# Kernel tuning notes

Measured on AMD Instinct MI355X. Metric: run time of the kernel, lower is better.

Reference implementation:

```python
import jax, jax.numpy as jnp
import numpy as np
from jax import lax


def binarize(x):
    # sign() binarization with straight-through estimator (identity backward),
    # matching the BNN .data in-place trick in BinarizeConv2d / bilinear.
    return x + lax.stop_gradient(jnp.sign(x) - x)


def maxpool2x2(x):
    # NCHW 2x2 max pool, stride 2
    return lax.reduce_window(x, -jnp.inf, lax.max,
                             (1, 1, 2, 2), (1, 1, 2, 2), 'VALID')


def conv2d(x, w):
    # NCHW / OIHW valid conv, stride 1
    return lax.conv_general_dilated(x, w, (1, 1), 'VALID',
                                    dimension_numbers=('NCHW', 'OIHW', 'NCHW'))


def setup_inputs() -> dict:
    key = jax.random.key(0)
    ks = jax.random.split(key, 6)
    B = 16384
    x = jax.random.normal(ks[0], (B, 1, 32, 32), dtype=jnp.float32)
    w1 = jax.random.normal(ks[1], (6, 1, 5, 5), dtype=jnp.float32) * 0.2
    w2 = jax.random.normal(ks[2], (16, 6, 5, 5), dtype=jnp.float32) * 0.08
    wfc1 = jax.random.normal(ks[3], (120, 400), dtype=jnp.float32) * 0.05
    wfc2 = jax.random.normal(ks[4], (84, 120), dtype=jnp.float32) * 0.09
    wfc3 = jax.random.normal(ks[5], (10, 84), dtype=jnp.float32) * 0.1
    return {'x': x, 'w1': w1, 'w2': w2, 'wfc1': wfc1, 'wfc2': wfc2, 'wfc3': wfc3}


def reference(x, w1, w2, wfc1, wfc2, wfc3):
    # conv1 (binarized input + weights) -> pool
    h = maxpool2x2(conv2d(binarize(x), binarize(w1)))          # [B,6,14,14]
    # conv2 -> pool
    h = maxpool2x2(conv2d(binarize(h), binarize(w2)))          # [B,16,5,5]
    h = h.reshape(h.shape[0], -1)                              # [B,400]
    h = binarize(h) @ binarize(wfc1).T                         # [B,120]
    h = binarize(h) @ binarize(wfc2).T                         # [B,84]
    h = binarize(h) @ binarize(wfc3).T                         # [B,10]
    return h
```

## Files before the change

### kernel.cpp

```cpp
#include <hip/hip_runtime.h>
#include <hip/hip_bf16.h>

typedef unsigned int u32;
typedef unsigned short u16;
typedef unsigned long long u64;

#define OC1 0
#define OC2 8
#define WCONV 104
#define OF1 104
#define OF2 2024
#define OF3 2664
#define WTOT 2704

__global__ void pack_w(const float* __restrict__ w1, const float* __restrict__ w2,
                       const float* __restrict__ f1, const float* __restrict__ f2,
                       const float* __restrict__ f3, u64* __restrict__ P) {
    int g = blockIdx.x * 256 + threadIdx.x;
    if (g < 1920) {
        int j = g / 15, w = g % 15;
        u64 v = 0;
        if (w < 14 && j < 120) {
            bool sp = (w >= 7); int k = sp ? w - 7 : w;
            for (int f = 0; f < 4; f++) {
                int p = 4 * k + f;
                if (p < 25)
                    for (int ch = 0; ch < 16; ch++) {
                        float x = f1[j * 400 + ch * 25 + p];
                        bool b = sp ? (x < 0.0f) : (x != 0.0f);
                        if (b) v |= 1ull << (f * 16 + ch);
                    }
            }
        }
        P[OF1 + g] = v;
    } else if (g < 2560) {
        int g2 = g - 1920, j = g2 / 5, w = g2 % 5;
        u64 v = 0;
        if (w < 4 && j < 84) {
            bool sp = (w >= 2); int h = w & 1;
            for (int b = 0; b < 64; b++) {
                int k = h * 64 + b;
                if (k < 120) {
                    float x = f2[j * 120 + k];
                    bool bb = sp ? (x < 0.0f) : (x != 0.0f);
                    if (bb) v |= 1ull << b;
                }
            }
        }
        P[OF2 + g2] = v;
    } else if (g < 2600) {
        int g3 = g - 2560, j = g3 / 4, w = g3 % 4;
        bool sp = (w >= 2); int h = w & 1;
        u64 v = 0;
        for (int b = 0; b < 64; b++) {
            int k = h * 64 + b;
            if (k < 84) {
                float x = f3[j * 84 + k];
                bool bb = sp ? (x < 0.0f) : (x != 0.0f);
                if (bb) v |= 1ull << b;
            }
        }
        P[OF3 + g3] = v;
    } else if (g < 2696) {
        int c = g - 2600, ch = c / 6, w = c % 6;
        bool sp = (w >= 3); int wp = w % 3;
        u64 v = 0;
        for (int half = 0; half < 2; half++) {
            int r = 2 * wp + half;
            if (r < 5) {
                u32 rowv = 0;
                for (int ci = 0; ci < 6; ci++)
                    for (int cc = 0; cc < 5; cc++) {
                        float x = w2[((ch * 6 + ci) * 5 + r) * 5 + cc];
                        bool b = sp ? (x < 0.0f) : (x != 0.0f);
                        int bit = (ci < 3) ? (5 * ci + cc) : (15 + 5 * (ci - 3) + cc);
                        if (b) rowv |= 1u << bit;
                    }
                v |= (u64)rowv << (32 * half);
            }
        }
        P[OC2 + ch * 6 + (sp ? 3 : 0) + wp] = v;
    } else if (g < 2702) {
        int c = g - 2696;
        int pair = c % 3; bool sp = (c >= 3);
        u64 v = 0;
        for (int half = 0; half < 2; half++) {
            int ch = 2 * pair + half;
            u32 wd = 0;
            for (int r = 0; r < 5; r++)
                for (int cc = 0; cc < 5; cc++) {
                    float x = w1[ch * 25 + r * 5 + cc];
                    bool b = sp ? (x < 0.0f) : (x != 0.0f);
                    if (b) wd |= 1u << (6 * r + cc);
                }
            v |= (u64)wd << (32 * half);
        }
        P[OC1 + (sp ? 3 : 0) + pair] = v;
    }
}

#define G 8

__device__ __forceinline__ u32 sgnb(int v) { return (u32)v >> 31; }
__device__ __forceinline__ u32 nzb(int v)  { return (u32)(v | -v) >> 31; }
#define WB() __builtin_amdgcn_wave_barrier()

__global__ __launch_bounds__(256, 8) void lenet_main(const float* __restrict__ X,
                                                     const u64* __restrict__ P,
                                                     float* __restrict__ out) {
    __shared__ u32 xs[G][32], xn[G][32];
    __shared__ u64 h1An[G][14], h1As[G][14], h1Bn[G][14], h1Bs[G][14];
    __shared__ u64 h2n[G][7], h2s[G][7];
    __shared__ u64 f1s[G][2], f1n[G][2], f2s[G][2], f2n[G][2];

    const int tid = threadIdx.x;
    const int wid = tid >> 6, lane = tid & 63;
    const int img0 = blockIdx.x * G;
    const int li0 = wid * 2;

    u64 zb = 0;
    {
        const float4* X4 = (const float4*)(X + (size_t)img0 * 1024);
        for (int it = 0; it < 8; it++) {
            int li = li0 + (it >> 2);
            int f4 = ((it & 3) << 6) + lane;
            float4 v = X4[li * 256 + f4];
            u32 s = (v.x < 0.0f ? 1u : 0u) | (v.y < 0.0f ? 2u : 0u)
                  | (v.z < 0.0f ? 4u : 0u) | (v.w < 0.0f ? 8u : 0u);
            u32 n = (v.x != 0.0f ? 1u : 0u) | (v.y != 0.0f ? 2u : 0u)
                  | (v.z != 0.0f ? 4u : 0u) | (v.w != 0.0f ? 8u : 0u);
            zb |= __ballot(n != 15u);
            int pos = 4 * (f4 & 7);
            u32 sw = s << pos, nw = n << pos;
            sw |= __shfl_xor((int)sw, 1); sw |= __shfl_xor((int)sw, 2); sw |= __shfl_xor((int)sw, 4);
            nw |= __shfl_xor((int)nw, 1); nw |= __shfl_xor((int)nw, 2); nw |= __shfl_xor((int)nw, 4);
            if ((lane & 7) == 0) { xs[li][f4 >> 3] = sw; xn[li][f4 >> 3] = nw; }
        }
    }
    u64 db;
    {
        bool bad = false;
        if (lane < 51) {
            u64 w, exp;
            if (lane < 48) {
                int ch = lane / 3, k = lane % 3;
                w = P[OC2 + ch * 6 + k];
                exp = (k < 2) ? 0x3FFFFFFF3FFFFFFFull : 0x000000003FFFFFFFull;
            } else {
                w = P[OC1 + (lane - 48)];
                exp = 0x1F7DF7DF1F7DF7DFull;
            }
            bad = (w != exp);
        }
        db = __ballot(bad);
    }
    const bool fastp = ((zb | db) == 0);
    WB();

    {
        const int px = lane & 15;
        const int pxe = px < 14 ? px : 13;
        if (fastp) {
            u64 c1s[3];
            for (int p = 0; p < 3; p++) c1s[p] = P[OC1 + 3 + p];
            for (int it = 0; it < 7; it++) {
                int seg = it * 4 + (lane >> 4);
                int im = seg >= 14 ? 1 : 0, py = seg - 14 * im, li = li0 + im;
                int oy = 2 * py;
                u32 rs[6];
                for (int k = 0; k < 6; k++) rs[k] = xs[li][oy + k];
                u32 cnt[6];
                for (int c = 0; c < 6; c++) cnt[c] = 255;
                for (int dx = 0; dx < 2; dx++) {
                    int t2 = 2 * pxe + dx;
                    u32 w0 = 0;
                    for (int r = 0; r < 5; r++) w0 |= ((rs[r] >> t2) & 31u) << (6 * r);
                    u32 w1 = (w0 >> 6) | (((rs[5] >> t2) & 31u) << 24);
                    for (int dy = 0; dy < 2; dy++) {
                        u32 w = dy ? w1 : w0;
                        u64 W = ((u64)w << 32) | w;
                        for (int p = 0; p < 3; p++) {
                            u64 t = W ^ c1s[p];
                            cnt[2 * p]     = min(cnt[2 * p],     (u32)__popc((u32)t));
                            cnt[2 * p + 1] = min(cnt[2 * p + 1], (u32)__popc((u32)(t >> 32)));
                        }
                    }
                }
                u64 bS[6];
                for (int c = 0; c < 6; c++) bS[c] = __ballot(cnt[c] >= 13);
                if (px == 0) {
                    int sh = lane & 48;
                    u64 rAs = ((bS[0] >> sh) & 0x3FFF) | (((bS[1] >> sh) & 0x3FFF) << 16) | (((bS[2] >> sh) & 0x3FFF) << 32);
                    u64 rBs = ((bS[3] >> sh) & 0x3FFF) | (((bS[4] >> sh) & 0x3FFF) << 16) | (((bS[5] >> sh) & 0x3FFF) << 32);
                    h1As[li][py] = rAs; h1Bs[li][py] = rBs;
                }
            }
        } else {
            u64 c1n[3], c1s[3];
            for (int p = 0; p < 3; p++) { c1n[p] = P[OC1 + p]; c1s[p] = P[OC1 + 3 + p]; }
            for (int it = 0; it < 7; it++) {
                int seg = it * 4 + (lane >> 4);
                int im = seg >= 14 ? 1 : 0, py = seg - 14 * im, li = li0 + im;
                int oy = 2 * py;
                u32 rn[6], rs[6];
                for (int k = 0; k < 6; k++) { rn[k] = xn[li][oy + k]; rs[k] = xs[li][oy + k]; }
                int best[6];
                for (int c = 0; c < 6; c++) best[c] = -1000;
                for (int dx = 0; dx < 2; dx++) {
                    int t2 = 2 * pxe + dx;
                    u32 wn0 = 0, ws0 = 0;
                    for (int r = 0; r < 5; r++) {
                        wn0 |= ((rn[r] >> t2) & 31u) << (6 * r);
                        ws0 |= ((rs[r] >> t2) & 31u) << (6 * r);
                    }
                    u32 wn1 = (wn0 >> 6) | (((rn[5] >> t2) & 31u) << 24);
                    u32 ws1 = (ws0 >> 6) | (((rs[5] >> t2) & 31u) << 24);
                    for (int dy = 0; dy < 2; dy++) {
                        u32 wn = dy ? wn1 : wn0, ws = dy ? ws1 : ws0;
                        u64 Wn = ((u64)wn << 32) | wn;
                        u64 Ws = ((u64)ws << 32) | ws;
                        for (int p = 0; p < 3; p++) {
                            u64 m  = Wn & c1n[p];
                            u64 mx = m & (Ws ^ c1s[p]);
                            int a0 = __popc((u32)m) - 2 * __popc((u32)mx);
                            int a1 = __popc((u32)(m >> 32)) - 2 * __popc((u32)(mx >> 32));
                            best[2 * p]     = max(best[2 * p], a0);
                            best[2 * p + 1] = max(best[2 * p + 1], a1);
                        }
                    }
                }
                u64 bS[6], bN[6];
                for (int c = 0; c < 6; c++) {
                    bS[c] = __ballot(best[c] < 0);
                    bN[c] = __ballot(best[c] != 0);
                }
                if (px == 0) {
                    int sh = lane & 48;
                    u64 rAs = ((bS[0] >> sh) & 0x3FFF) | (((bS[1] >> sh) & 0x3FFF) << 16) | (((bS[2] >> sh) & 0x3FFF) << 32);
                    u64 rAn = ((bN[0] >> sh) & 0x3FFF) | (((bN[1] >> sh) & 0x3FFF) << 16) | (((bN[2] >> sh) & 0x3FFF) << 32);
                    u64 rBs = ((bS[3] >> sh) & 0x3FFF) | (((bS[4] >> sh) & 0x3FFF) << 16) | (((bS[5] >> sh) & 0x3FFF) << 32);
                    u64 rBn = ((bN[3] >> sh) & 0x3FFF) | (((bN[4] >> sh) & 0x3FFF) << 16) | (((bN[5] >> sh) & 0x3FFF) << 32);
                    h1As[li][py] = rAs; h1An[li][py] = rAn;
                    h1Bs[li][py] = rBs; h1Bn[li][py] = rBn;
                }
            }
        }
    }
    WB();

    if (lane < 6) {
        int li = li0 + (lane >= 3 ? 1 : 0); int t = lane % 3;
        ((u16*)h2n[li])[25 + t] = 0; ((u16*)h2s[li])[25 + t] = 0;
    }
    if (fastp) {
        if (lane < 50) {
            int im = lane >= 25 ? 1 : 0, p = lane - 25 * im, li = li0 + im;
            int py = p / 5, px2 = p % 5;
            int y0 = 2 * py;
            u32 dsg[2][6];
            for (int r = 0; r < 6; r++) {
                u64 a = h1As[li][y0 + r], b = h1Bs[li][y0 + r];
                for (int dx = 0; dx < 2; dx++) {
                    int t2 = 2 * px2 + dx;
                    u64 as = a >> t2, bs = b >> t2;
                    dsg[dx][r] = (((u32)as & 31u) | ((u32)(as >> 11) & 0x3E0u) | ((u32)(as >> 22) & 0x7C00u))
                               | ((((u32)bs & 31u) | ((u32)(bs >> 11) & 0x3E0u) | ((u32)(bs >> 22) & 0x7C00u)) << 15);
                }
            }
            u64 Ps[2][4];
            for (int dx = 0; dx < 2; dx++)
                for (int r = 0; r < 4; r++)
                    Ps[dx][r] = (u64)dsg[dx][r] | ((u64)dsg[dx][r + 1] << 32);
            u32 sb = 0, nb = 0;
            #pragma unroll 4
            for (int ch = 0; ch < 16; ch++) {
                u64 w0s = P[OC2 + ch * 6 + 3], w1s = P[OC2 + ch * 6 + 4];
                u32 w2s = (u32)P[OC2 + ch * 6 + 5];
                u32 mn = 255;
                for (int dy = 0; dy < 2; dy++)
                    for (int dx = 0; dx < 2; dx++) {
                        u64 t0 = Ps[dx][dy] ^ w0s, t1 = Ps[dx][dy + 2] ^ w1s;
                        u32 t2v = (dy ? dsg[dx][5] : dsg[dx][4]) ^ w2s;
                        u32 c = __popcll(t0) + __popcll(t1) + __popc(t2v);
                        mn = min(mn, c);
                    }
                sb |= (mn >= 76 ? 1u : 0u) << ch;
                nb |= (mn != 75 ? 1u : 0u) << ch;
            }
            ((u16*)h2s[li])[p] = (u16)sb;
            ((u16*)h2n[li])[p] = (u16)nb;
        }
    } else {
        if (lane < 50) {
            int im = lane >= 25 ? 1 : 0, p = lane - 25 * im, li = li0 + im;
            int py = p / 5, px2 = p % 5;
            int y0 = 2 * py;
            u32 dn[2][6], dsg[2][6];
            for (int r = 0; r < 6; r++) {
                u64 a_n = h1An[li][y0 + r], a_s = h1As[li][y0 + r];
                u64 b_n = h1Bn[li][y0 + r], b_s = h1Bs[li][y0 + r];
                for (int dx = 0; dx < 2; dx++) {
                    int t2 = 2 * px2 + dx;
                    u64 an = a_n >> t2, as = a_s >> t2, bn = b_n >> t2, bs = b_s >> t2;
                    dn[dx][r]  = (((u32)an & 31u) | ((u32)(an >> 11) & 0x3E0u) | ((u32)(an >> 22) & 0x7C00u))
                               | ((((u32)bn & 31u) | ((u32)(bn >> 11) & 0x3E0u) | ((u32)(bn >> 22) & 0x7C00u)) << 15);
                    dsg[dx][r] = (((u32)as & 31u) | ((u32)(as >> 11) & 0x3E0u) | ((u32)(as >> 22) & 0x7C00u))
                               | ((((u32)bs & 31u) | ((u32)(bs >> 11) & 0x3E0u) | ((u32)(bs >> 22) & 0x7C00u)) << 15);
                }
            }
            u64 Pn[2][4], Ps[2][4];
            for (int dx = 0; dx < 2; dx++)
                for (int r = 0; r < 4; r++) {
                    Pn[dx][r] = (u64)dn[dx][r]  | ((u64)dn[dx][r + 1]  << 32);
                    Ps[dx][r] = (u64)dsg[dx][r] | ((u64)dsg[dx][r + 1] << 32);
                }
            u32 sb = 0, nb = 0;
            #pragma unroll 4
            for (int ch = 0; ch < 16; ch++) {
                u64 w0n = P[OC2 + ch * 6 + 0], w1n = P[OC2 + ch * 6 + 1];
                u32 w2n = (u32)P[OC2 + ch * 6 + 2];
                u64 w0s = P[OC2 + ch * 6 + 3], w1s = P[OC2 + ch * 6 + 4];
                u32 w2s = (u32)P[OC2 + ch * 6 + 5];
                int am = -1000000;
                for (int dy = 0; dy < 2; dy++)
                    for (int dx = 0; dx < 2; dx++) {
                        u64 m0 = Pn[dx][dy] & w0n, m1 = Pn[dx][dy + 2] & w1n;
                        u32 m2 = (dy ? dn[dx][5] : dn[dx][4]) & w2n;
                        u64 x0 = m0 & (Ps[dx][dy] ^ w0s), x1 = m1 & (Ps[dx][dy + 2] ^ w1s);
                        u32 x2 = m2 & ((dy ? dsg[dx][5] : dsg[dx][4]) ^ w2s);
                        int v = __popcll(m0) + __popcll(m1) + __popc(m2)
                              - 2 * (__popcll(x0) + __popcll(x1) + __popc(x2));
                        am = max(am, v);
                    }
                sb |= sgnb(am) << ch;
                nb |= nzb(am) << ch;
            }
            ((u16*)h2s[li])[p] = (u16)sb;
            ((u16*)h2n[li])[p] = (u16)nb;
        }
    }
    WB();

    for (int it = 0; it < 4; it++) {
        int im = it >> 1, word = it & 1, li = li0 + im;
        int j = word * 64 + lane;
        const u64* wj = P + OF1 + j * 15;
        int acc = 0;
        for (int k = 0; k < 7; k++) {
            u64 m  = h2n[li][k] & wj[k];
            u64 mx = m & (h2s[li][k] ^ wj[7 + k]);
            acc += __popcll(m) - 2 * __popcll(mx);
        }
        u64 bs = __ballot(acc < 0);
        u64 bn = __ballot(acc != 0);
        if (lane == 0) { f1s[li][word] = bs; f1n[li][word] = bn; }
    }
    WB();

    for (int it = 0; it < 4; it++) {
        int im = it >> 1, word = it & 1, li = li0 + im;
        int j = word * 64 + lane;
        const u64* wj = P + OF2 + j * 5;
        u64 m0 = f1n[li][0] & wj[0], m1 = f1n[li][1] & wj[1];
        u64 x0 = m0 & (f1s[li][0] ^ wj[2]), x1 = m1 & (f1s[li][1] ^ wj[3]);
        int acc = __popcll(m0) + __popcll(m1) - 2 * (__popcll(x0) + __popcll(x1));
        u64 bs = __ballot(acc < 0);
        u64 bn = __ballot(acc != 0);
        if (lane == 0) { f2s[li][word] = bs; f2n[li][word] = bn; }
    }
    WB();

    if (lane < 32) {
        int im = lane >> 4, j = lane & 15, li = li0 + im;
        if (j < 10) {
            const u64* wj = P + OF3 + j * 4;
            u64 m0 = f2n[li][0] & wj[0], m1 = f2n[li][1] & wj[1];
            u64 x0 = m0 & (f2s[li][0] ^ wj[2]), x1 = m1 & (f2s[li][1] ^ wj[3]);
            int acc = __popcll(m0) + __popcll(m1) - 2 * (__popcll(x0) + __popcll(x1));
            out[(size_t)(img0 + li) * 10 + j] = (float)acc;
        }
    }
}

extern "C" void kernel_launch(void* const* d_in, const int* in_sizes, int n_in,
                              void* d_out, int out_size, void* d_ws, size_t ws_size,
                              hipStream_t stream) {
    const float* x    = (const float*)d_in[0];
    const float* w1   = (const float*)d_in[1];
    const float* w2   = (const float*)d_in[2];
    const float* wfc1 = (const float*)d_in[3];
    const float* wfc2 = (const float*)d_in[4];
    const float* wfc3 = (const float*)d_in[5];
    float* out = (float*)d_out;
    u64* P = (u64*)d_ws;

    int B = in_sizes[0] / 1024;

    pack_w<<<11, 256, 0, stream>>>(w1, w2, wfc1, wfc2, wfc3, P);
    lenet_main<<<B / G, 256, 0, stream>>>(x, P, out);
}
```

Baseline: 146.6 us.

## Pipeline per-image input loads with conv1 and decide fast path per image

Each wavefront now handles its two images in sequence. It issues the second image's float4 loads before running conv1 on the first, so global-load latency overlaps with compute. The fast/slow path decision is made per image, and the non-zero bitmasks are built only when an image needs the slow path. Conv1 window extraction is simplified by extracting a 6-bit window once and masking it for both dx offsets. FC1 and FC2 weights are loaded once per word and reused across both images. The cost is more register pressure from the held float4s and duplicated code.

Measured after the change: 168.7 us. +15.1%, slower.

```diff
diff --git a/kernel.cpp b/kernel.cpp
--- a/kernel.cpp
+++ b/kernel.cpp
@@ -116,27 +116,15 @@
     const int tid = threadIdx.x;
     const int wid = tid >> 6, lane = tid & 63;
     const int img0 = blockIdx.x * G;
-    const int li0 = wid * 2;
-
-    u64 zb = 0;
-    {
-        const float4* X4 = (const float4*)(X + (size_t)img0 * 1024);
-        for (int it = 0; it < 8; it++) {
-            int li = li0 + (it >> 2);
-            int f4 = ((it & 3) << 6) + lane;
-            float4 v = X4[li * 256 + f4];
-            u32 s = (v.x < 0.0f ? 1u : 0u) | (v.y < 0.0f ? 2u : 0u)
-                  | (v.z < 0.0f ? 4u : 0u) | (v.w < 0.0f ? 8u : 0u);
-            u32 n = (v.x != 0.0f ? 1u : 0u) | (v.y != 0.0f ? 2u : 0u)
-                  | (v.z != 0.0f ? 4u : 0u) | (v.w != 0.0f ? 8u : 0u);
-            zb |= __ballot(n != 15u);
-            int pos = 4 * (f4 & 7);
-            u32 sw = s << pos, nw = n << pos;
-            sw |= __shfl_xor((int)sw, 1); sw |= __shfl_xor((int)sw, 2); sw |= __shfl_xor((int)sw, 4);
-            nw |= __shfl_xor((int)nw, 1); nw |= __shfl_xor((int)nw, 2); nw |= __shfl_xor((int)nw, 4);
-            if ((lane & 7) == 0) { xs[li][f4 >> 3] = sw; xn[li][f4 >> 3] = nw; }
-        }
-    }
+    const int liA = wid * 2, liB = liA + 1;
+    const int li0 = liA;
+
+    const float4* X4 = (const float4*)(X + (size_t)img0 * 1024);
+
+    float4 rvA[4];
+    #pragma unroll
+    for (int it = 0; it < 4; it++) rvA[it] = X4[liA * 256 + it * 64 + lane];
+
     u64 db;
     {
         bool bad = false;
@@ -154,109 +142,177 @@
         }
         db = __ballot(bad);
     }
-    const bool fastp = ((zb | db) == 0);
-    WB();
-
-    {
+
+    auto conv1_fast = [&](int li) {
         const int px = lane & 15;
         const int pxe = px < 14 ? px : 13;
-        if (fastp) {
-            u64 c1s[3];
-            for (int p = 0; p < 3; p++) c1s[p] = P[OC1 + 3 + p];
-            for (int it = 0; it < 7; it++) {
-                int seg = it * 4 + (lane >> 4);
-                int im = seg >= 14 ? 1 : 0, py = seg - 14 * im, li = li0 + im;
-                int oy = 2 * py;
-                u32 rs[6];
-                for (int k = 0; k < 6; k++) rs[k] = xs[li][oy + k];
-                u32 cnt[6];
-                for (int c = 0; c < 6; c++) cnt[c] = 255;
+        const int tt = 2 * pxe;
+        const int g = lane >> 4;
+        u64 c1s0 = P[OC1 + 3], c1s1 = P[OC1 + 4], c1s2 = P[OC1 + 5];
+        #pragma unroll
+        for (int it = 0; it < 4; it++) {
+            int seg = it * 4 + g;
+            int py = seg < 14 ? seg : 13;
+            int oy = 2 * py;
+            u32 rs[6];
+            #pragma unroll
+            for (int k = 0; k < 6; k++) rs[k] = xs[li][oy + k];
+            u32 W6a = 0;
+            #pragma unroll
+            for (int r = 0; r < 5; r++) W6a |= ((rs[r] >> tt) & 63u) << (6 * r);
+            u32 W6b = (W6a >> 6) | (((rs[5] >> tt) & 63u) << 24);
+            u32 cnt[6];
+            #pragma unroll
+            for (int c = 0; c < 6; c++) cnt[c] = 255;
+            #pragma unroll
+            for (int dy = 0; dy < 2; dy++) {
+                u32 base = dy ? W6b : W6a;
+                #pragma unroll
                 for (int dx = 0; dx < 2; dx++) {
-                    int t2 = 2 * pxe + dx;
-                    u32 w0 = 0;
-                    for (int r = 0; r < 5; r++) w0 |= ((rs[r] >> t2) & 31u) << (6 * r);
-                    u32 w1 = (w0 >> 6) | (((rs[5] >> t2) & 31u) << 24);
-                    for (int dy = 0; dy < 2; dy++) {
-                        u32 w = dy ? w1 : w0;
-                        u64 W = ((u64)w << 32) | w;
-                        for (int p = 0; p < 3; p++) {
-                            u64 t = W ^ c1s[p];
-                            cnt[2 * p]     = min(cnt[2 * p],     (u32)__popc((u32)t));
-                            cnt[2 * p + 1] = min(cnt[2 * p + 1], (u32)__popc((u32)(t >> 32)));
-                        }
-                    }
-                }
-                u64 bS[6];
-                for (int c = 0; c < 6; c++) bS[c] = __ballot(cnt[c] >= 13);
-                if (px == 0) {
-                    int sh = lane & 48;
-                    u64 rAs = ((bS[0] >> sh) & 0x3FFF) | (((bS[1] >> sh) & 0x3FFF) << 16) | (((bS[2] >> sh) & 0x3FFF) << 32);
-                    u64 rBs = ((bS[3] >> sh) & 0x3FFF) | (((bS[4] >> sh) & 0x3FFF) << 16) | (((bS[5] >> sh) & 0x3FFF) << 32);
-                    h1As[li][py] = rAs; h1Bs[li][py] = rBs;
-                }
-            }
-        } else {
-            u64 c1n[3], c1s[3];
-            for (int p = 0; p < 3; p++) { c1n[p] = P[OC1 + p]; c1s[p] = P[OC1 + 3 + p]; }
-            for (int it = 0; it < 7; it++) {
-                int seg = it * 4 + (lane >> 4);
-                int im = seg >= 14 ? 1 : 0, py = seg - 14 * im, li = li0 + im;
-                int oy = 2 * py;
-                u32 rn[6], rs[6];
-                for (int k = 0; k < 6; k++) { rn[k] = xn[li][oy + k]; rs[k] = xs[li][oy + k]; }
-                int best[6];
-                for (int c = 0; c < 6; c++) best[c] = -1000;
+                    u32 w = (dx ? (base >> 1) : base) & 0x1F7DF7DFu;
+                    u64 W = ((u64)w << 32) | w;
+                    u64 t0 = W ^ c1s0;
+                    cnt[0] = min(cnt[0], (u32)__popc((u32)t0));
+                    cnt[1] = min(cnt[1], (u32)__popc((u32)(t0 >> 32)));
+                    u64 t1 = W ^ c1s1;
+                    cnt[2] = min(cnt[2], (u32)__popc((u32)t1));
+                    cnt[3] = min(cnt[3], (u32)__popc((u32)(t1 >> 32)));
+                    u64 t2w = W ^ c1s2;
+                    cnt[4] = min(cnt[4], (u32)__popc((u32)t2w));
+                    cnt[5] = min(cnt[5], (u32)__popc((u32)(t2w >> 32)));
+                }
+            }
+            u64 bS[6];
+            #pragma unroll
+            for (int c = 0; c < 6; c++) bS[c] = __ballot(cnt[c] >= 13);
+            if (px == 0 && seg < 14) {
+                int sh = lane & 48;
+                u64 rAs = ((bS[0] >> sh) & 0x3FFF) | (((bS[1] >> sh) & 0x3FFF) << 16) | (((bS[2] >> sh) & 0x3FFF) << 32);
+                u64 rBs = ((bS[3] >> sh) & 0x3FFF) | (((bS[4] >> sh) & 0x3FFF) << 16) | (((bS[5] >> sh) & 0x3FFF) << 32);
+                h1As[li][seg] = rAs; h1Bs[li][seg] = rBs;
+            }
+        }
+    };
+    auto conv1_slow = [&](int li) {
+        const int px = lane & 15;
+        const int pxe = px < 14 ? px : 13;
+        const int tt = 2 * pxe;
+        const int g = lane >> 4;
+        for (int it = 0; it < 4; it++) {
+            int seg = it * 4 + g;
+            int py = seg < 14 ? seg : 13;
+            int oy = 2 * py;
+            int best[6];
+            for (int c = 0; c < 6; c++) best[c] = -1000;
+            for (int dy = 0; dy < 2; dy++)
                 for (int dx = 0; dx < 2; dx++) {
-                    int t2 = 2 * pxe + dx;
-                    u32 wn0 = 0, ws0 = 0;
+                    u32 wn = 0, ws = 0;
                     for (int r = 0; r < 5; r++) {
-                        wn0 |= ((rn[r] >> t2) & 31u) << (6 * r);
-                        ws0 |= ((rs[r] >> t2) & 31u) << (6 * r);
-                    }
-                    u32 wn1 = (wn0 >> 6) | (((rn[5] >> t2) & 31u) << 24);
-                    u32 ws1 = (ws0 >> 6) | (((rs[5] >> t2) & 31u) << 24);
-                    for (int dy = 0; dy < 2; dy++) {
-                        u32 wn = dy ? wn1 : wn0, ws = dy ? ws1 : ws0;
-                        u64 Wn = ((u64)wn << 32) | wn;
-                        u64 Ws = ((u64)ws << 32) | ws;
-                        for (int p = 0; p < 3; p++) {
-                            u64 m  = Wn & c1n[p];
-                            u64 mx = m & (Ws ^ c1s[p]);
-                            int a0 = __popc((u32)m) - 2 * __popc((u32)mx);
-                            int a1 = __popc((u32)(m >> 32)) - 2 * __popc((u32)(mx >> 32));
-                            best[2 * p]     = max(best[2 * p], a0);
-                            best[2 * p + 1] = max(best[2 * p + 1], a1);
-                        }
-                    }
-                }
-                u64 bS[6], bN[6];
-                for (int c = 0; c < 6; c++) {
-                    bS[c] = __ballot(best[c] < 0);
-                    bN[c] = __ballot(best[c] != 0);
-                }
-                if (px == 0) {
-                    int sh = lane & 48;
-                    u64 rAs = ((bS[0] >> sh) & 0x3FFF) | (((bS[1] >> sh) & 0x3FFF) << 16) | (((bS[2] >> sh) & 0x3FFF) << 32);
-                    u64 rAn = ((bN[0] >> sh) & 0x3FFF) | (((bN[1] >> sh) & 0x3FFF) << 16) | (((bN[2] >> sh) & 0x3FFF) << 32);
-                    u64 rBs = ((bS[3] >> sh) & 0x3FFF) | (((bS[4] >> sh) & 0x3FFF) << 16) | (((bS[5] >> sh) & 0x3FFF) << 32);
-                    u64 rBn = ((bN[3] >> sh) & 0x3FFF) | (((bN[4] >> sh) & 0x3FFF) << 16) | (((bN[5] >> sh) & 0x3FFF) << 32);
-                    h1As[li][py] = rAs; h1An[li][py] = rAn;
-                    h1Bs[li][py] = rBs; h1Bn[li][py] = rBn;
-                }
-            }
-        }
-    }
+                        u32 an = xn[li][oy + dy + r], as = xs[li][oy + dy + r];
+                        wn |= ((an >> (tt + dx)) & 31u) << (6 * r);
+                        ws |= ((as >> (tt + dx)) & 31u) << (6 * r);
+                    }
+                    u64 Wn = ((u64)wn << 32) | wn;
+                    u64 Ws = ((u64)ws << 32) | ws;
+                    for (int p = 0; p < 3; p++) {
+                        u64 cn = P[OC1 + p], cs = P[OC1 + 3 + p];
+                        u64 m  = Wn & cn;
+                        u64 mx = m & (Ws ^ cs);
+                        int a0 = __popc((u32)m) - 2 * __popc((u32)mx);
+                        int a1 = __popc((u32)(m >> 32)) - 2 * __popc((u32)(mx >> 32));
+                        best[2 * p]     = max(best[2 * p], a0);
+                        best[2 * p + 1] = max(best[2 * p + 1], a1);
+                    }
+                }
+            u64 bS[6], bN[6];
+            for (int c = 0; c < 6; c++) {
+                bS[c] = __ballot(best[c] < 0);
+                bN[c] = __ballot(best[c] != 0);
+            }
+            if (px == 0 && seg < 14) {
+                int sh = lane & 48;
+                u64 rAs = ((bS[0] >> sh) & 0x3FFF) | (((bS[1] >> sh) & 0x3FFF) << 16) | (((bS[2] >> sh) & 0x3FFF) << 32);
+                u64 rAn = ((bN[0] >> sh) & 0x3FFF) | (((bN[1] >> sh) & 0x3FFF) << 16) | (((bN[2] >> sh) & 0x3FFF) << 32);
+                u64 rBs = ((bS[3] >> sh) & 0x3FFF) | (((bS[4] >> sh) & 0x3FFF) << 16) | (((bS[5] >> sh) & 0x3FFF) << 32);
+                u64 rBn = ((bN[3] >> sh) & 0x3FFF) | (((bN[4] >> sh) & 0x3FFF) << 16) | (((bN[5] >> sh) & 0x3FFF) << 32);
+                h1As[li][seg] = rAs; h1An[li][seg] = rAn;
+                h1Bs[li][seg] = rBs; h1Bn[li][seg] = rBn;
+            }
+        }
+    };
+
+    u32 naccA = 15u;
+    #pragma unroll
+    for (int it = 0; it < 4; it++) {
+        float4 v = rvA[it];
+        u32 s = (v.x < 0.0f ? 1u : 0u) | (v.y < 0.0f ? 2u : 0u)
+              | (v.z < 0.0f ? 4u : 0u) | (v.w < 0.0f ? 8u : 0u);
+        u32 n = (v.x != 0.0f ? 1u : 0u) | (v.y != 0.0f ? 2u : 0u)
+              | (v.z != 0.0f ? 4u : 0u) | (v.w != 0.0f ? 8u : 0u);
+        naccA &= n;
+        u32 sw = s << (4 * (lane & 7));
+        sw |= __shfl_xor((int)sw, 1); sw |= __shfl_xor((int)sw, 2); sw |= __shfl_xor((int)sw, 4);
+        if ((lane & 7) == 0) xs[liA][it * 8 + (lane >> 3)] = sw;
+    }
+    const bool fpA = ((__ballot(naccA != 15u) | db) == 0);
+    if (!fpA) {
+        #pragma unroll
+        for (int it = 0; it < 4; it++) {
+            float4 v = rvA[it];
+            u32 n = (v.x != 0.0f ? 1u : 0u) | (v.y != 0.0f ? 2u : 0u)
+                  | (v.z != 0.0f ? 4u : 0u) | (v.w != 0.0f ? 8u : 0u);
+            u32 nw = n << (4 * (lane & 7));
+            nw |= __shfl_xor((int)nw, 1); nw |= __shfl_xor((int)nw, 2); nw |= __shfl_xor((int)nw, 4);
+            if ((lane & 7) == 0) xn[liA][it * 8 + (lane >> 3)] = nw;
+        }
+    }
+
+    float4 rvB[4];
+    #pragma unroll
+    for (int it = 0; it < 4; it++) rvB[it] = X4[liB * 256 + it * 64 + lane];
+
+    WB();
+    if (fpA) conv1_fast(liA); else conv1_slow(liA);
+
+    u32 naccB = 15u;
+    #pragma unroll
+    for (int it = 0; it < 4; it++) {
+        float4 v = rvB[it];
+        u32 s = (v.x < 0.0f ? 1u : 0u) | (v.y < 0.0f ? 2u : 0u)
+              | (v.z < 0.0f ? 4u : 0u) | (v.w < 0.0f ? 8u : 0u);
+        u32 n = (v.x != 0.0f ? 1u : 0u) | (v.y != 0.0f ? 2u : 0u)
+              | (v.z != 0.0f ? 4u : 0u) | (v.w != 0.0f ? 8u : 0u);
+        naccB &= n;
+        u32 sw = s << (4 * (lane & 7));
+        sw |= __shfl_xor((int)sw, 1); sw |= __shfl_xor((int)sw, 2); sw |= __shfl_xor((int)sw, 4);
+        if ((lane & 7) == 0) xs[liB][it * 8 + (lane >> 3)] = sw;
+    }
+    const bool fpB = ((__ballot(naccB != 15u) | db) == 0);
+    if (!fpB) {
+        #pragma unroll
+        for (int it = 0; it < 4; it++) {
+            float4 v = rvB[it];
+            u32 n = (v.x != 0.0f ? 1u : 0u) | (v.y != 0.0f ? 2u : 0u)
+                  | (v.z != 0.0f ? 4u : 0u) | (v.w != 0.0f ? 8u : 0u);
+            u32 nw = n << (4 * (lane & 7));
+            nw |= __shfl_xor((int)nw, 1); nw |= __shfl_xor((int)nw, 2); nw |= __shfl_xor((int)nw, 4);
+            if ((lane & 7) == 0) xn[liB][it * 8 + (lane >> 3)] = nw;
+        }
+    }
+    WB();
+    if (fpB) conv1_fast(liB); else conv1_slow(liB);
     WB();
 
     if (lane < 6) {
         int li = li0 + (lane >= 3 ? 1 : 0); int t = lane % 3;
         ((u16*)h2n[li])[25 + t] = 0; ((u16*)h2s[li])[25 + t] = 0;
     }
-    if (fastp) {
-        if (lane < 50) {
-            int im = lane >= 25 ? 1 : 0, p = lane - 25 * im, li = li0 + im;
-            int py = p / 5, px2 = p % 5;
-            int y0 = 2 * py;
+    if (lane < 50) {
+        int im = lane >= 25 ? 1 : 0, p = lane - 25 * im, li = li0 + im;
+        bool cfast = im ? fpB : fpA;
+        int py = p / 5, px2 = p % 5;
+        int y0 = 2 * py;
+        if (cfast) {
             u32 dsg[2][6];
             for (int r = 0; r < 6; r++) {
                 u64 a = h1As[li][y0 + r], b = h1Bs[li][y0 + r];
@@ -289,12 +345,7 @@
             }
             ((u16*)h2s[li])[p] = (u16)sb;
             ((u16*)h2n[li])[p] = (u16)nb;
-        }
-    } else {
-        if (lane < 50) {
-            int im = lane >= 25 ? 1 : 0, p = lane - 25 * im, li = li0 + im;
-            int py = p / 5, px2 = p % 5;
-            int y0 = 2 * py;
+        } else {
             u32 dn[2][6], dsg[2][6];
             for (int r = 0; r < 6; r++) {
                 u64 a_n = h1An[li][y0 + r], a_s = h1As[li][y0 + r];
@@ -341,32 +392,45 @@
     }
     WB();
 
-    for (int it = 0; it < 4; it++) {
-        int im = it >> 1, word = it & 1, li = li0 + im;
+    #pragma unroll
+    for (int word = 0; word < 2; word++) {
         int j = word * 64 + lane;
         const u64* wj = P + OF1 + j * 15;
-        int acc = 0;
-        for (int k = 0; k < 7; k++) {
-            u64 m  = h2n[li][k] & wj[k];
-            u64 mx = m & (h2s[li][k] ^ wj[7 + k]);
-            acc += __popcll(m) - 2 * __popcll(mx);
-        }
-        u64 bs = __ballot(acc < 0);
-        u64 bn = __ballot(acc != 0);
-        if (lane == 0) { f1s[li][word] = bs; f1n[li][word] = bn; }
-    }
-    WB();
-
-    for (int it = 0; it < 4; it++) {
-        int im = it >> 1, word = it & 1, li = li0 + im;
+        u64 wn[7], ws[7];
+        #pragma unroll
+        for (int k = 0; k < 7; k++) { wn[k] = wj[k]; ws[k] = wj[7 + k]; }
+        #pragma unroll
+        for (int im = 0; im < 2; im++) {
+            int li = li0 + im;
+            int acc = 0;
+            #pragma unroll
+            for (int k = 0; k < 7; k++) {
+                u64 m  = h2n[li][k] & wn[k];
+                u64 mx = m & (h2s[li][k] ^ ws[k]);
+                acc += __popcll(m) - 2 * __popcll(mx);
+            }
+            u64 bs = __ballot(acc < 0);
+            u64 bn = __ballot(acc != 0);
+            if (lane == 0) { f1s[li][word] = bs; f1n[li][word] = bn; }
+        }
+    }
+    WB();
+
+    #pragma unroll
+    for (int word = 0; word < 2; word++) {
         int j = word * 64 + lane;
         const u64* wj = P + OF2 + j * 5;
-        u64 m0 = f1n[li][0] & wj[0], m1 = f1n[li][1] & wj[1];
-        u64 x0 = m0 & (f1s[li][0] ^ wj[2]), x1 = m1 & (f1s[li][1] ^ wj[3]);
-        int acc = __popcll(m0) + __popcll(m1) - 2 * (__popcll(x0) + __popcll(x1));
-        u64 bs = __ballot(acc < 0);
-        u64 bn = __ballot(acc != 0);
-        if (lane == 0) { f2s[li][word] = bs; f2n[li][word] = bn; }
+        u64 a0 = wj[0], a1 = wj[1], s0 = wj[2], s1 = wj[3];
+        #pragma unroll
+        for (int im = 0; im < 2; im++) {
+            int li = li0 + im;
+            u64 m0 = f1n[li][0] & a0, m1 = f1n[li][1] & a1;
+            u64 x0 = m0 & (f1s[li][0] ^ s0), x1 = m1 & (f1s[li][1] ^ s1);
+            int acc = __popcll(m0) + __popcll(m1) - 2 * (__popcll(x0) + __popcll(x1));
+            u64 bs = __ballot(acc < 0);
+            u64 bn = __ballot(acc != 0);
+            if (lane == 0) { f2s[li][word] = bs; f2n[li][word] = bn; }
+        }
     }
     WB();
 
```

## Defer nonzero-mask packing to slow path and streamline conv1 window extraction

Applied to the files above, without the earlier changes.

The input-packing loop now builds only the sign bitmask and tracks nonzero-ness with a cheap per-lane AND. The nonzero mask is computed by re-reading X only when the zero-free fast path is rejected. The fast conv1 loop extracts a 6-bit window once per row and derives both dx offsets by shift and mask, with scalarized accumulators and full unrolling. The fc1/fc2 loops load each weight row once and reuse it for both images. The slow path re-reads shared memory and global weights inside its loops to save registers, which makes that path more expensive.

Measured after the change: 180.6 us. 23.2% more time.

```diff
diff --git a/kernel.cpp b/kernel.cpp
--- a/kernel.cpp
+++ b/kernel.cpp
@@ -118,24 +118,22 @@
     const int img0 = blockIdx.x * G;
     const int li0 = wid * 2;
 
-    u64 zb = 0;
-    {
-        const float4* X4 = (const float4*)(X + (size_t)img0 * 1024);
-        for (int it = 0; it < 8; it++) {
-            int li = li0 + (it >> 2);
-            int f4 = ((it & 3) << 6) + lane;
-            float4 v = X4[li * 256 + f4];
-            u32 s = (v.x < 0.0f ? 1u : 0u) | (v.y < 0.0f ? 2u : 0u)
-                  | (v.z < 0.0f ? 4u : 0u) | (v.w < 0.0f ? 8u : 0u);
-            u32 n = (v.x != 0.0f ? 1u : 0u) | (v.y != 0.0f ? 2u : 0u)
-                  | (v.z != 0.0f ? 4u : 0u) | (v.w != 0.0f ? 8u : 0u);
-            zb |= __ballot(n != 15u);
-            int pos = 4 * (f4 & 7);
-            u32 sw = s << pos, nw = n << pos;
-            sw |= __shfl_xor((int)sw, 1); sw |= __shfl_xor((int)sw, 2); sw |= __shfl_xor((int)sw, 4);
-            nw |= __shfl_xor((int)nw, 1); nw |= __shfl_xor((int)nw, 2); nw |= __shfl_xor((int)nw, 4);
-            if ((lane & 7) == 0) { xs[li][f4 >> 3] = sw; xn[li][f4 >> 3] = nw; }
-        }
+    const float4* X4 = (const float4*)(X + (size_t)img0 * 1024);
+
+    u32 nacc = 15u;
+    #pragma unroll
+    for (int it = 0; it < 8; it++) {
+        int li = li0 + (it >> 2);
+        int f4 = ((it & 3) << 6) + lane;
+        float4 v = X4[li * 256 + f4];
+        u32 s = (v.x < 0.0f ? 1u : 0u) | (v.y < 0.0f ? 2u : 0u)
+              | (v.z < 0.0f ? 4u : 0u) | (v.w < 0.0f ? 8u : 0u);
+        u32 n = (v.x != 0.0f ? 1u : 0u) | (v.y != 0.0f ? 2u : 0u)
+              | (v.z != 0.0f ? 4u : 0u) | (v.w != 0.0f ? 8u : 0u);
+        nacc &= n;
+        u32 sw = s << (4 * (lane & 7));
+        sw |= __shfl_xor((int)sw, 1); sw |= __shfl_xor((int)sw, 2); sw |= __shfl_xor((int)sw, 4);
+        if ((lane & 7) == 0) xs[li][f4 >> 3] = sw;
     }
     u64 db;
     {
@@ -154,81 +152,93 @@
         }
         db = __ballot(bad);
     }
-    const bool fastp = ((zb | db) == 0);
+    const bool fastp = ((__ballot(nacc != 15u) | db) == 0);
+    if (!fastp) {
+        for (int it = 0; it < 8; it++) {
+            int li = li0 + (it >> 2);
+            int f4 = ((it & 3) << 6) + lane;
+            float4 v = X4[li * 256 + f4];
+            u32 n = (v.x != 0.0f ? 1u : 0u) | (v.y != 0.0f ? 2u : 0u)
+                  | (v.z != 0.0f ? 4u : 0u) | (v.w != 0.0f ? 8u : 0u);
+            u32 nw = n << (4 * (lane & 7));
+            nw |= __shfl_xor((int)nw, 1); nw |= __shfl_xor((int)nw, 2); nw |= __shfl_xor((int)nw, 4);
+            if ((lane & 7) == 0) xn[li][f4 >> 3] = nw;
+        }
+    }
     WB();
 
     {
         const int px = lane & 15;
         const int pxe = px < 14 ? px : 13;
+        const int tt = 2 * pxe;
         if (fastp) {
-            u64 c1s[3];
-            for (int p = 0; p < 3; p++) c1s[p] = P[OC1 + 3 + p];
+            u64 c1s0 = P[OC1 + 3], c1s1 = P[OC1 + 4], c1s2 = P[OC1 + 5];
+            #pragma unroll
             for (int it = 0; it < 7; it++) {
                 int seg = it * 4 + (lane >> 4);
                 int im = seg >= 14 ? 1 : 0, py = seg - 14 * im, li = li0 + im;
                 int oy = 2 * py;
-                u32 rs[6];
-                for (int k = 0; k < 6; k++) rs[k] = xs[li][oy + k];
-                u32 cnt[6];
-                for (int c = 0; c < 6; c++) cnt[c] = 255;
-                for (int dx = 0; dx < 2; dx++) {
-                    int t2 = 2 * pxe + dx;
-                    u32 w0 = 0;
-                    for (int r = 0; r < 5; r++) w0 |= ((rs[r] >> t2) & 31u) << (6 * r);
-                    u32 w1 = (w0 >> 6) | (((rs[5] >> t2) & 31u) << 24);
-                    for (int dy = 0; dy < 2; dy++) {
-                        u32 w = dy ? w1 : w0;
+                u32 rs0 = xs[li][oy],     rs1 = xs[li][oy + 1], rs2 = xs[li][oy + 2];
+                u32 rs3 = xs[li][oy + 3], rs4 = xs[li][oy + 4], rs5 = xs[li][oy + 5];
+                u32 W6a = ((rs0 >> tt) & 63u) | (((rs1 >> tt) & 63u) << 6)
+                        | (((rs2 >> tt) & 63u) << 12) | (((rs3 >> tt) & 63u) << 18)
+                        | (((rs4 >> tt) & 63u) << 24);
+                u32 W6b = (W6a >> 6) | (((rs5 >> tt) & 63u) << 24);
+                u32 c0 = 255, c1 = 255, c2 = 255, c3 = 255, c4 = 255, c5 = 255;
+                #pragma unroll
+                for (int dy = 0; dy < 2; dy++) {
+                    u32 base = dy ? W6b : W6a;
+                    #pragma unroll
+                    for (int dx = 0; dx < 2; dx++) {
+                        u32 w = (dx ? (base >> 1) : base) & 0x1F7DF7DFu;
                         u64 W = ((u64)w << 32) | w;
-                        for (int p = 0; p < 3; p++) {
-                            u64 t = W ^ c1s[p];
-                            cnt[2 * p]     = min(cnt[2 * p],     (u32)__popc((u32)t));
-                            cnt[2 * p + 1] = min(cnt[2 * p + 1], (u32)__popc((u32)(t >> 32)));
-                        }
-                    }
-                }
-                u64 bS[6];
-                for (int c = 0; c < 6; c++) bS[c] = __ballot(cnt[c] >= 13);
+                        u64 t0 = W ^ c1s0;
+                        c0 = min(c0, (u32)__popc((u32)t0));
+                        c1 = min(c1, (u32)__popc((u32)(t0 >> 32)));
+                        u64 t1 = W ^ c1s1;
+                        c2 = min(c2, (u32)__popc((u32)t1));
+                        c3 = min(c3, (u32)__popc((u32)(t1 >> 32)));
+                        u64 t2 = W ^ c1s2;
+                        c4 = min(c4, (u32)__popc((u32)t2));
+                        c5 = min(c5, (u32)__popc((u32)(t2 >> 32)));
+                    }
+                }
+                u64 b0 = __ballot(c0 >= 13), b1 = __ballot(c1 >= 13);
+                u64 b2 = __ballot(c2 >= 13), b3 = __ballot(c3 >= 13);
+                u64 b4 = __ballot(c4 >= 13), b5 = __ballot(c5 >= 13);
                 if (px == 0) {
                     int sh = lane & 48;
-                    u64 rAs = ((bS[0] >> sh) & 0x3FFF) | (((bS[1] >> sh) & 0x3FFF) << 16) | (((bS[2] >> sh) & 0x3FFF) << 32);
-                    u64 rBs = ((bS[3] >> sh) & 0x3FFF) | (((bS[4] >> sh) & 0x3FFF) << 16) | (((bS[5] >> sh) & 0x3FFF) << 32);
-                    h1As[li][py] = rAs; h1Bs[li][py] = rBs;
+                    h1As[li][py] = ((b0 >> sh) & 0x3FFF) | (((b1 >> sh) & 0x3FFF) << 16) | (((b2 >> sh) & 0x3FFF) << 32);
+                    h1Bs[li][py] = ((b3 >> sh) & 0x3FFF) | (((b4 >> sh) & 0x3FFF) << 16) | (((b5 >> sh) & 0x3FFF) << 32);
                 }
             }
         } else {
-            u64 c1n[3], c1s[3];
-            for (int p = 0; p < 3; p++) { c1n[p] = P[OC1 + p]; c1s[p] = P[OC1 + 3 + p]; }
             for (int it = 0; it < 7; it++) {
                 int seg = it * 4 + (lane >> 4);
                 int im = seg >= 14 ? 1 : 0, py = seg - 14 * im, li = li0 + im;
                 int oy = 2 * py;
-                u32 rn[6], rs[6];
-                for (int k = 0; k < 6; k++) { rn[k] = xn[li][oy + k]; rs[k] = xs[li][oy + k]; }
                 int best[6];
                 for (int c = 0; c < 6; c++) best[c] = -1000;
-                for (int dx = 0; dx < 2; dx++) {
-                    int t2 = 2 * pxe + dx;
-                    u32 wn0 = 0, ws0 = 0;
-                    for (int r = 0; r < 5; r++) {
-                        wn0 |= ((rn[r] >> t2) & 31u) << (6 * r);
-                        ws0 |= ((rs[r] >> t2) & 31u) << (6 * r);
-                    }
-                    u32 wn1 = (wn0 >> 6) | (((rn[5] >> t2) & 31u) << 24);
-                    u32 ws1 = (ws0 >> 6) | (((rs[5] >> t2) & 31u) << 24);
-                    for (int dy = 0; dy < 2; dy++) {
-                        u32 wn = dy ? wn1 : wn0, ws = dy ? ws1 : ws0;
+                for (int dy = 0; dy < 2; dy++)
+                    for (int dx = 0; dx < 2; dx++) {
+                        u32 wn = 0, ws = 0;
+                        for (int r = 0; r < 5; r++) {
+                            u32 an = xn[li][oy + dy + r], as = xs[li][oy + dy + r];
+                            wn |= ((an >> (tt + dx)) & 31u) << (6 * r);
+                            ws |= ((as >> (tt + dx)) & 31u) << (6 * r);
+                        }
                         u64 Wn = ((u64)wn << 32) | wn;
                         u64 Ws = ((u64)ws << 32) | ws;
                         for (int p = 0; p < 3; p++) {
-                            u64 m  = Wn & c1n[p];
-                            u64 mx = m & (Ws ^ c1s[p]);
+                            u64 cn = P[OC1 + p], cs = P[OC1 + 3 + p];
+                            u64 m  = Wn & cn;
+                            u64 mx = m & (Ws ^ cs);
                             int a0 = __popc((u32)m) - 2 * __popc((u32)mx);
                             int a1 = __popc((u32)(m >> 32)) - 2 * __popc((u32)(mx >> 32));
                             best[2 * p]     = max(best[2 * p], a0);
                             best[2 * p + 1] = max(best[2 * p + 1], a1);
                         }
                     }
-                }
                 u64 bS[6], bN[6];
                 for (int c = 0; c < 6; c++) {
                     bS[c] = __ballot(best[c] < 0);
@@ -236,12 +246,10 @@
                 }
                 if (px == 0) {
                     int sh = lane & 48;
-                    u64 rAs = ((bS[0] >> sh) & 0x3FFF) | (((bS[1] >> sh) & 0x3FFF) << 16) | (((bS[2] >> sh) & 0x3FFF) << 32);
-                    u64 rAn = ((bN[0] >> sh) & 0x3FFF) | (((bN[1] >> sh) & 0x3FFF) << 16) | (((bN[2] >> sh) & 0x3FFF) << 32);
-                    u64 rBs = ((bS[3] >> sh) & 0x3FFF) | (((bS[4] >> sh) & 0x3FFF) << 16) | (((bS[5] >> sh) & 0x3FFF) << 32);
-                    u64 rBn = ((bN[3] >> sh) & 0x3FFF) | (((bN[4] >> sh) & 0x3FFF) << 16) | (((bN[5] >> sh) & 0x3FFF) << 32);
-                    h1As[li][py] = rAs; h1An[li][py] = rAn;
-                    h1Bs[li][py] = rBs; h1Bn[li][py] = rBn;
+                    h1As[li][py] = ((bS[0] >> sh) & 0x3FFF) | (((bS[1] >> sh) & 0x3FFF) << 16) | (((bS[2] >> sh) & 0x3FFF) << 32);
+                    h1An[li][py] = ((bN[0] >> sh) & 0x3FFF) | (((bN[1] >> sh) & 0x3FFF) << 16) | (((bN[2] >> sh) & 0x3FFF) << 32);
+                    h1Bs[li][py] = ((bS[3] >> sh) & 0x3FFF) | (((bS[4] >> sh) & 0x3FFF) << 16) | (((bS[5] >> sh) & 0x3FFF) << 32);
+                    h1Bn[li][py] = ((bN[3] >> sh) & 0x3FFF) | (((bN[4] >> sh) & 0x3FFF) << 16) | (((bN[5] >> sh) & 0x3FFF) << 32);
                 }
             }
         }
@@ -341,32 +349,45 @@
     }
     WB();
 
-    for (int it = 0; it < 4; it++) {
-        int im = it >> 1, word = it & 1, li = li0 + im;
+    #pragma unroll
+    for (int word = 0; word < 2; word++) {
         int j = word * 64 + lane;
         const u64* wj = P + OF1 + j * 15;
-        int acc = 0;
-        for (int k = 0; k < 7; k++) {
-            u64 m  = h2n[li][k] & wj[k];
-            u64 mx = m & (h2s[li][k] ^ wj[7 + k]);
-            acc += __popcll(m) - 2 * __popcll(mx);
-        }
-        u64 bs = __ballot(acc < 0);
-        u64 bn = __ballot(acc != 0);
-        if (lane == 0) { f1s[li][word] = bs; f1n[li][word] = bn; }
+        u64 wn[7], ws[7];
+        #pragma unroll
+        for (int k = 0; k < 7; k++) { wn[k] = wj[k]; ws[k] = wj[7 + k]; }
+        #pragma unroll
+        for (int im = 0; im < 2; im++) {
+            int li = li0 + im;
+            int acc = 0;
+            #pragma unroll
+            for (int k = 0; k < 7; k++) {
+                u64 m  = h2n[li][k] & wn[k];
+                u64 mx = m & (h2s[li][k] ^ ws[k]);
+                acc += __popcll(m) - 2 * __popcll(mx);
+            }
+            u64 bs = __ballot(acc < 0);
+            u64 bn = __ballot(acc != 0);
+            if (lane == 0) { f1s[li][word] = bs; f1n[li][word] = bn; }
+        }
     }
     WB();
 
-    for (int it = 0; it < 4; it++) {
-        int im = it >> 1, word = it & 1, li = li0 + im;
+    #pragma unroll
+    for (int word = 0; word < 2; word++) {
         int j = word * 64 + lane;
         const u64* wj = P + OF2 + j * 5;
-        u64 m0 = f1n[li][0] & wj[0], m1 = f1n[li][1] & wj[1];
-        u64 x0 = m0 & (f1s[li][0] ^ wj[2]), x1 = m1 & (f1s[li][1] ^ wj[3]);
-        int acc = __popcll(m0) + __popcll(m1) - 2 * (__popcll(x0) + __popcll(x1));
-        u64 bs = __ballot(acc < 0);
-        u64 bn = __ballot(acc != 0);
-        if (lane == 0) { f2s[li][word] = bs; f2n[li][word] = bn; }
+        u64 a0 = wj[0], a1 = wj[1], s0 = wj[2], s1 = wj[3];
+        #pragma unroll
+        for (int im = 0; im < 2; im++) {
+            int li = li0 + im;
+            u64 m0 = f1n[li][0] & a0, m1 = f1n[li][1] & a1;
+            u64 x0 = m0 & (f1s[li][0] ^ s0), x1 = m1 & (f1s[li][1] ^ s1);
+            int acc = __popcll(m0) + __popcll(m1) - 2 * (__popcll(x0) + __popcll(x1));
+            u64 bs = __ballot(acc < 0);
+            u64 bn = __ballot(acc != 0);
+            if (lane == 0) { f2s[li][word] = bs; f2n[li][word] = bn; }
+        }
     }
     WB();
 
```
